# Kernel tuning notes

Measured on AMD Instinct MI355X. Metric: run time of the kernel, lower is better.

Reference implementation:

```python
import jax, jax.numpy as jnp
import numpy as np

NC, NX, NY = 32, 512, 512
N_LOC = 100000


def setup_inputs() -> dict:
    key = jax.random.key(0)
    k1, k2 = jax.random.split(key)
    x = jax.random.normal(k1, (8, NC, NX, NY), dtype=jnp.float32)
    kernel = jnp.zeros((1, NC, NX, NY), dtype=jnp.float32)
    variable_kernel = jax.random.normal(k2, (N_LOC,), dtype=jnp.float32)
    # unique flat indices into the (NC, NX, NY) kernel volume (cluster locations)
    rng = np.random.default_rng(0)
    loc_idx = jnp.asarray(rng.choice(NC * NX * NY, N_LOC, replace=False).astype(np.int64))
    return {"x": x, "kernel": kernel, "variable_kernel": variable_kernel, "loc_idx": loc_idx}


def fill_kernel(kernel, variable_kernel, loc_idx):
    # scatter ReLU'd trainable values into the sparse PSF locations
    k0 = kernel[0].reshape(-1).at[loc_idx].set(jax.nn.relu(variable_kernel))
    return k0.reshape(NC, NX, NY)


def disperse_all_orders(x, k):
    # per-channel circular convolution with the multi-order dispersion PSF,
    # summed over spectral channels onto the sensor: (b, nx, ny)
    Xf = jnp.fft.rfft2(x, axes=(-2, -1))          # (b, nc, nx, ny//2+1)
    Kf = jnp.fft.rfft2(k, axes=(-2, -1))          # (nc, nx, ny//2+1)
    Yf = jnp.sum(Xf * Kf[None], axis=1)           # (b, nx, ny//2+1)
    return jnp.fft.irfft2(Yf, s=(NX, NY), axes=(-2, -1))


def reference(x, kernel, variable_kernel, loc_idx):
    k = fill_kernel(kernel, variable_kernel, loc_idx)
    return disperse_all_orders(x, k)
```

## Files before the change

### kernel.cpp

```cpp
#include <hip/hip_runtime.h>
#include <cstdint>

#define NXX 512
#define NYY 512
#define NCH 32
#define NB  8
#define NU  257
#define IMG_CPLX (NU*NXX)
#define PIX (NXX*NYY)

__device__ __forceinline__ uint32_t f2bf(float f){
  uint32_t u = __float_as_uint(f);
  return (u + 0x7FFFu + ((u >> 16) & 1u)) >> 16;
}
__device__ __forceinline__ float bf2f(uint32_t h){ return __uint_as_float(h << 16); }
__device__ __forceinline__ uint32_t packbf(float re, float im){ return f2bf(re) | (f2bf(im) << 16); }

#define WAIT_LGKM() asm volatile("s_waitcnt lgkmcnt(0)" ::: "memory")

__device__ __forceinline__ void cmul(float& zr, float& zi, float wr, float wi){
  float r = zr*wr - zi*wi;
  zi = zr*wi + zi*wr;
  zr = r;
}

template<int DIR>
__device__ __forceinline__ void bfly8(float* xr, float* xi){
  const float S = 0.70710678118654752440f;
  float er0=xr[0]+xr[4], ei0=xi[0]+xi[4];
  float er1=xr[1]+xr[5], ei1=xi[1]+xi[5];
  float er2=xr[2]+xr[6], ei2=xi[2]+xi[6];
  float er3=xr[3]+xr[7], ei3=xi[3]+xi[7];
  float or0=xr[0]-xr[4], oi0=xi[0]-xi[4];
  float or1=xr[1]-xr[5], oi1=xi[1]-xi[5];
  float or2=xr[2]-xr[6], oi2=xi[2]-xi[6];
  float or3=xr[3]-xr[7], oi3=xi[3]-xi[7];
  float p0r=er0+er2, p0i=ei0+ei2;
  float p1r=er0-er2, p1i=ei0-ei2;
  float q0r=er1+er3, q0i=ei1+ei3;
  float q1r=er1-er3, q1i=ei1-ei3;
  float w4r, w4i;
  if (DIR<0){ w4r=q1i; w4i=-q1r; } else { w4r=-q1i; w4i=q1r; }
  xr[0]=p0r+q0r; xi[0]=p0i+q0i;
  xr[4]=p0r-q0r; xi[4]=p0i-q0i;
  xr[2]=p1r+w4r; xi[2]=p1i+w4i;
  xr[6]=p1r-w4r; xi[6]=p1i-w4i;
  float f1r,f1i,f2r,f2i,f3r,f3i;
  if (DIR<0){
    f1r=S*(or1+oi1); f1i=S*(oi1-or1);
    f2r=oi2;         f2i=-or2;
    f3r=S*(oi3-or3); f3i=-S*(or3+oi3);
  } else {
    f1r=S*(or1-oi1);  f1i=S*(or1+oi1);
    f2r=-oi2;         f2i=or2;
    f3r=-S*(or3+oi3); f3i=S*(or3-oi3);
  }
  float g0r=or0+f2r, g0i=oi0+f2i;
  float g1r=or0-f2r, g1i=oi0-f2i;
  float h0r=f1r+f3r, h0i=f1i+f3i;
  float h1r=f1r-f3r, h1i=f1i-f3i;
  float v4r, v4i;
  if (DIR<0){ v4r=h1i; v4i=-h1r; } else { v4r=-h1i; v4i=h1r; }
  xr[1]=g0r+h0r; xi[1]=g0i+h0i;
  xr[5]=g0r-h0r; xi[5]=g0i-h0i;
  xr[3]=g1r+v4r; xi[3]=g1i+v4i;
  xr[7]=g1r-v4r; xi[7]=g1i-v4i;
}

__device__ __forceinline__ void make_tw(int t, float* t1r, float* t1i, float* t2r, float* t2i){
  const float TP = 6.283185307179586476925f;
  float s, c;
  sincosf(-TP * (float)t * (1.0f/512.0f), &s, &c);
  t1r[0]=1.0f; t1i[0]=0.0f;
  #pragma unroll
  for (int k=1;k<8;k++){ t1r[k]=t1r[k-1]*c - t1i[k-1]*s; t1i[k]=t1r[k-1]*s + t1i[k-1]*c; }
  sincosf(-TP * (float)(t>>3) * (1.0f/64.0f), &s, &c);
  t2r[0]=1.0f; t2i[0]=0.0f;
  #pragma unroll
  for (int k=1;k<8;k++){ t2r[k]=t2r[k-1]*c - t2i[k-1]*s; t2i[k]=t2r[k-1]*s + t2i[k-1]*c; }
}

template<int DIR>
__device__ __forceinline__ void fft512(float* ar, float* ai, float* sre, float* sim, int t,
    const float* t1r, const float* t1i, const float* t2r, const float* t2i){
  bfly8<DIR>(ar, ai);
  #pragma unroll
  for (int k=1;k<8;k++){ cmul(ar[k], ai[k], t1r[k], (DIR<0)? t1i[k] : -t1i[k]); }
  #pragma unroll
  for (int k=0;k<8;k++){ int d = 8*t + k; d += (d>>5); sre[d]=ar[k]; sim[d]=ai[k]; }
  WAIT_LGKM();
  #pragma unroll
  for (int j=0;j<8;j++){ int s2 = t + (j<<6); s2 += (s2>>5); ar[j]=sre[s2]; ai[j]=sim[s2]; }
  WAIT_LGKM();
  bfly8<DIR>(ar, ai);
  #pragma unroll
  for (int k=1;k<8;k++){ cmul(ar[k], ai[k], t2r[k], (DIR<0)? t2i[k] : -t2i[k]); }
  #pragma unroll
  for (int k=0;k<8;k++){ int d = (t&7) + ((t>>3)<<6) + (k<<3); d += (d>>5); sre[d]=ar[k]; sim[d]=ai[k]; }
  WAIT_LGKM();
  #pragma unroll
  for (int j=0;j<8;j++){ int s2 = t + (j<<6); s2 += (s2>>5); ar[j]=sre[s2]; ai[j]=sim[s2]; }
  WAIT_LGKM();
  bfly8<DIR>(ar, ai);
}

__global__ __launch_bounds__(256) void k_zero(uint4* __restrict__ p, int n4){
  int stride = gridDim.x * 256;
  for (int i = blockIdx.x*256 + threadIdx.x; i < n4; i += stride)
    p[i] = make_uint4(0u,0u,0u,0u);
}

__global__ void k_scatter(const float* __restrict__ vk, const int* __restrict__ loc,
                          float* __restrict__ kbuf, int n){
  int i = blockIdx.x*256 + threadIdx.x;
  if (i < n){ float v = vk[i]; kbuf[loc[i]] = v > 0.0f ? v : 0.0f; }
}

__global__ __launch_bounds__(512) void k_p1(const float* __restrict__ src,
                                            uint32_t* __restrict__ dst){
  __shared__ float sre[8][528], sim[8][528];
  __shared__ uint32_t staged[NU*17];
  const int tid = threadIdx.x;
  const int w = tid >> 6, t = tid & 63;
  const int img = blockIdx.x >> 5;
  const int rblock = (blockIdx.x & 31) << 4;
  float t1r[8],t1i[8],t2r[8],t2i[8];
  make_tw(t, t1r,t1i,t2r,t2i);
  const float* rowA = src + (size_t)img*PIX + (size_t)(rblock + 2*w)*NYY;
  float ar[8], ai[8];
  #pragma unroll
  for (int j=0;j<8;j++){ ar[j]=rowA[t+(j<<6)]; ai[j]=rowA[NYY + t + (j<<6)]; }
  fft512<-1>(ar,ai,sre[w],sim[w],t,t1r,t1i,t2r,t2i);
  #pragma unroll
  for (int k=0;k<8;k++){ int d = t+(k<<6); d += (d>>5); sre[w][d]=ar[k]; sim[w][d]=ai[k]; }
  WAIT_LGKM();
  #pragma unroll
  for (int k=0;k<5;k++){
    int u = t + (k<<6);
    if (u < NU){
      int e2 = (512 - u) & 511;
      int du = u + (u>>5), d2 = e2 + (e2>>5);
      float zur=sre[w][du], zui=sim[w][du];
      float zvr=sre[w][d2], zvi=sim[w][d2];
      float Ar=0.5f*(zur+zvr), Ai=0.5f*(zui-zvi);
      float Br=0.5f*(zui+zvi), Bi=0.5f*(zvr-zur);
      staged[u*17 + 2*w]     = packbf(Ar,Ai);
      staged[u*17 + 2*w + 1] = packbf(Br,Bi);
    }
  }
  __syncthreads();
  uint32_t* ob = dst + (size_t)img*IMG_CPLX;
  for (int e = tid; e < NU*16; e += 512){
    int u = e >> 4, il = e & 15;
    ob[(size_t)u*NXX + rblock + il] = staged[u*17 + il];
  }
}

__global__ __launch_bounds__(512) void k_p2k(uint32_t* __restrict__ rtk){
  __shared__ float sre[8][528], sim[8][528];
  const int w = threadIdx.x >> 6, t = threadIdx.x & 63;
  const int fid = blockIdx.x*8 + w;
  const int c = fid / NU, u = fid % NU;
  float t1r[8],t1i[8],t2r[8],t2i[8];
  make_tw(t, t1r,t1i,t2r,t2i);
  uint32_t* col = rtk + (size_t)c*IMG_CPLX + (size_t)u*NXX;
  float ar[8], ai[8];
  #pragma unroll
  for (int j=0;j<8;j++){ uint32_t v = col[t+(j<<6)]; ar[j]=bf2f(v & 0xFFFFu); ai[j]=bf2f(v >> 16); }
  fft512<-1>(ar,ai,sre[w],sim[w],t,t1r,t1i,t2r,t2i);
  #pragma unroll
  for (int k=0;k<8;k++){ col[t+(k<<6)] = packbf(ar[k], ai[k]); }
}

__global__ __launch_bounds__(512) void k_p3(const uint32_t* __restrict__ rtx,
    const uint32_t* __restrict__ rtk, uint32_t* __restrict__ y3, int b0, int gsh){
  __shared__ float sre[8][528], sim[8][528];
  const int w = threadIdx.x >> 6, t = threadIdx.x & 63;
  const int G = 1 << gsh;
  const int u = blockIdx.x * (8 >> gsh) + (w >> gsh);
  const int bl = w & (G-1);
  if (u >= NU) return;
  float t1r[8],t1i[8],t2r[8],t2i[8];
  make_tw(t, t1r,t1i,t2r,t2i);
  float accr[8], acci[8];
  #pragma unroll
  for (int k=0;k<8;k++){ accr[k]=0.0f; acci[k]=0.0f; }
  for (int c=0;c<NCH;c++){
    const uint32_t* xc = rtx + ((size_t)(bl*NCH + c))*IMG_CPLX + (size_t)u*NXX;
    float ar[8], ai[8];
    #pragma unroll
    for (int j=0;j<8;j++){ uint32_t v = xc[t+(j<<6)]; ar[j]=bf2f(v & 0xFFFFu); ai[j]=bf2f(v >> 16); }
    fft512<-1>(ar,ai,sre[w],sim[w],t,t1r,t1i,t2r,t2i);
    const uint32_t* kc = rtk + (size_t)c*IMG_CPLX + (size_t)u*NXX;
    #pragma unroll
    for (int k=0;k<8;k++){
      uint32_t kv = kc[t+(k<<6)];
      float kr=bf2f(kv & 0xFFFFu), ki=bf2f(kv >> 16);
      accr[k] += ar[k]*kr - ai[k]*ki;
      acci[k] += ar[k]*ki + ai[k]*kr;
    }
  }
  const float sc = 1.0f/262144.0f;
  #pragma unroll
  for (int k=0;k<8;k++){ accr[k]*=sc; acci[k]*=sc; }
  fft512<1>(accr,acci,sre[w],sim[w],t,t1r,t1i,t2r,t2i);
  uint32_t* yc = y3 + ((size_t)(b0+bl)*NU + u)*NXX;
  #pragma unroll
  for (int k=0;k<8;k++){ yc[t+(k<<6)] = packbf(accr[k], acci[k]); }
}

__global__ __launch_bounds__(512) void k_p4(const uint32_t* __restrict__ y3,
                                            float* __restrict__ out){
  __shared__ float sre[8][528], sim[8][528];
  __shared__ uint32_t sta[NU*17];
  const int tid = threadIdx.x, w = tid>>6, t = tid&63;
  const int b = blockIdx.x >> 5;
  const int i0 = (blockIdx.x & 31) << 4;
  const uint32_t* yb = y3 + (size_t)b*IMG_CPLX;
  for (int e = tid; e < NU*16; e += 512){
    int u = e >> 4, il = e & 15;
    sta[u*17 + il] = yb[(size_t)u*NXX + i0 + il];
  }
  __syncthreads();
  float t1r[8],t1i[8],t2r[8],t2i[8];
  make_tw(t, t1r,t1i,t2r,t2i);
  float ar[8], ai[8];
  #pragma unroll
  for (int j=0;j<8;j++){
    int e = t + (j<<6);
    if (e <= 256){
      uint32_t pa_ = sta[e*17 + 2*w], pb_ = sta[e*17 + 2*w + 1];
      float Ar=bf2f(pa_&0xFFFFu), Ai=bf2f(pa_>>16);
      float Br=bf2f(pb_&0xFFFFu), Bi=bf2f(pb_>>16);
      ar[j] = Ar - Bi; ai[j] = Ai + Br;
    } else {
      int ep = 512 - e;
      uint32_t pa_ = sta[ep*17 + 2*w], pb_ = sta[ep*17 + 2*w + 1];
      float Ar=bf2f(pa_&0xFFFFu), Ai=bf2f(pa_>>16);
      float Br=bf2f(pb_&0xFFFFu), Bi=bf2f(pb_>>16);
      ar[j] = Ar + Bi; ai[j] = Br - Ai;
    }
  }
  fft512<1>(ar,ai,sre[w],sim[w],t,t1r,t1i,t2r,t2i);
  float* ob = out + (size_t)b*PIX + (size_t)(i0 + 2*w)*NYY;
  #pragma unroll
  for (int k=0;k<8;k++){ int n = t+(k<<6); ob[n]=ar[k]; ob[NYY+n]=ai[k]; }
}

extern "C" void kernel_launch(void* const* d_in, const int* in_sizes, int n_in,
                              void* d_out, int out_size, void* d_ws, size_t ws_size,
                              hipStream_t stream) {
  const float* x  = (const float*)d_in[0];
  const float* vk = (const float*)d_in[2];
  const int*   loc= (const int*)d_in[3];
  float* out = (float*)d_out;
  char* ws = (char*)d_ws;
  const int n_loc = in_sizes[2];

  const size_t kbytes   = (size_t)NCH*PIX*4;
  const size_t imgbytes = (size_t)IMG_CPLX*4;

  float*    kbuf = (float*)ws;
  uint32_t* y3   = (uint32_t*)ws;
  uint32_t* rtk  = (uint32_t*)(ws + kbytes);
  uint32_t* rtx  = rtk + (size_t)NCH*IMG_CPLX;

  int G = 8;
  while (G > 1 && kbytes + (size_t)(NCH + NCH*G)*imgbytes > ws_size) G >>= 1;
  const int gsh = (G==8)?3:((G==4)?2:((G==2)?1:0));

  k_zero<<<2048, 256, 0, stream>>>((uint4*)kbuf, (int)(kbytes/16));
  k_scatter<<<(n_loc+255)/256, 256, 0, stream>>>(vk, loc, kbuf, n_loc);
  k_p1<<<NCH*32, 512, 0, stream>>>(kbuf, rtk);
  k_p2k<<<(NCH*NU)/8, 512, 0, stream>>>(rtk);
  for (int b0 = 0; b0 < NB; b0 += G){
    k_p1<<<G*NCH*32, 512, 0, stream>>>(x + (size_t)b0*NCH*PIX, rtx);
    const int upw = 8 >> gsh;
    const int nwg = (NU + upw - 1) / upw;
    k_p3<<<nwg, 512, 0, stream>>>(rtx, rtk, y3, b0, gsh);
  }
  k_p4<<<NB*32, 512, 0, stream>>>(y3, out);
}
```

Baseline: 210.9 us.

## Split channel loop across waves in k_p3 and widen k_p1 row tiles

The frequency-domain multiply-accumulate kernel now assigns one block per (column, batch) pair. Its eight waves each handle four channels, and an LDS reduction combines them before a single wave performs the inverse column FFT. This exposes far more blocks than the previous layout, where each wave serially looped over all 32 channels. The row FFT kernel now processes 32 rows per block in two passes, giving wider contiguous transposed writes. The cost is extra shared memory for the reduction buffers and an inverse-FFT tail where seven waves sit idle.

```diff
diff --git a/kernel.cpp b/kernel.cpp
--- a/kernel.cpp
+++ b/kernel.cpp
@@ -119,40 +119,45 @@
 __global__ __launch_bounds__(512) void k_p1(const float* __restrict__ src,
                                             uint32_t* __restrict__ dst){
   __shared__ float sre[8][528], sim[8][528];
-  __shared__ uint32_t staged[NU*17];
+  __shared__ uint32_t staged[NU*33];
   const int tid = threadIdx.x;
   const int w = tid >> 6, t = tid & 63;
-  const int img = blockIdx.x >> 5;
-  const int rblock = (blockIdx.x & 31) << 4;
+  const int img = blockIdx.x >> 4;
+  const int rblock = (blockIdx.x & 15) << 5;
   float t1r[8],t1i[8],t2r[8],t2i[8];
   make_tw(t, t1r,t1i,t2r,t2i);
-  const float* rowA = src + (size_t)img*PIX + (size_t)(rblock + 2*w)*NYY;
-  float ar[8], ai[8];
-  #pragma unroll
-  for (int j=0;j<8;j++){ ar[j]=rowA[t+(j<<6)]; ai[j]=rowA[NYY + t + (j<<6)]; }
-  fft512<-1>(ar,ai,sre[w],sim[w],t,t1r,t1i,t2r,t2i);
-  #pragma unroll
-  for (int k=0;k<8;k++){ int d = t+(k<<6); d += (d>>5); sre[w][d]=ar[k]; sim[w][d]=ai[k]; }
-  WAIT_LGKM();
-  #pragma unroll
-  for (int k=0;k<5;k++){
-    int u = t + (k<<6);
-    if (u < NU){
-      int e2 = (512 - u) & 511;
-      int du = u + (u>>5), d2 = e2 + (e2>>5);
-      float zur=sre[w][du], zui=sim[w][du];
-      float zvr=sre[w][d2], zvi=sim[w][d2];
-      float Ar=0.5f*(zur+zvr), Ai=0.5f*(zui-zvi);
-      float Br=0.5f*(zui+zvi), Bi=0.5f*(zvr-zur);
-      staged[u*17 + 2*w]     = packbf(Ar,Ai);
-      staged[u*17 + 2*w + 1] = packbf(Br,Bi);
+  #pragma unroll
+  for (int p=0; p<2; p++){
+    const int il = (w<<2) + (p<<1);
+    const float* rowA = src + (size_t)img*PIX + (size_t)(rblock + il)*NYY;
+    float ar[8], ai[8];
+    #pragma unroll
+    for (int j=0;j<8;j++){ ar[j]=rowA[t+(j<<6)]; ai[j]=rowA[NYY + t + (j<<6)]; }
+    fft512<-1>(ar,ai,sre[w],sim[w],t,t1r,t1i,t2r,t2i);
+    #pragma unroll
+    for (int k=0;k<8;k++){ int d = t+(k<<6); d += (d>>5); sre[w][d]=ar[k]; sim[w][d]=ai[k]; }
+    WAIT_LGKM();
+    #pragma unroll
+    for (int k=0;k<5;k++){
+      int u = t + (k<<6);
+      if (u < NU){
+        int e2 = (512 - u) & 511;
+        int du = u + (u>>5), d2 = e2 + (e2>>5);
+        float zur=sre[w][du], zui=sim[w][du];
+        float zvr=sre[w][d2], zvi=sim[w][d2];
+        float Ar=0.5f*(zur+zvr), Ai=0.5f*(zui-zvi);
+        float Br=0.5f*(zui+zvi), Bi=0.5f*(zvr-zur);
+        staged[u*33 + il]     = packbf(Ar,Ai);
+        staged[u*33 + il + 1] = packbf(Br,Bi);
+      }
     }
+    WAIT_LGKM();
   }
   __syncthreads();
   uint32_t* ob = dst + (size_t)img*IMG_CPLX;
-  for (int e = tid; e < NU*16; e += 512){
-    int u = e >> 4, il = e & 15;
-    ob[(size_t)u*NXX + rblock + il] = staged[u*17 + il];
+  for (int e = tid; e < NU*32; e += 512){
+    int u = e >> 5, il2 = e & 31;
+    ob[(size_t)u*NXX + rblock + il2] = staged[u*33 + il2];
   }
 }
 
@@ -175,38 +180,53 @@
 __global__ __launch_bounds__(512) void k_p3(const uint32_t* __restrict__ rtx,
     const uint32_t* __restrict__ rtk, uint32_t* __restrict__ y3, int b0, int gsh){
   __shared__ float sre[8][528], sim[8][528];
-  const int w = threadIdx.x >> 6, t = threadIdx.x & 63;
-  const int G = 1 << gsh;
-  const int u = blockIdx.x * (8 >> gsh) + (w >> gsh);
-  const int bl = w & (G-1);
-  if (u >= NU) return;
+  __shared__ float redr[8][512], redi[8][512];
+  const int tid = threadIdx.x;
+  const int w = tid >> 6, t = tid & 63;
+  const int u  = blockIdx.x >> gsh;
+  const int bl = blockIdx.x & ((1<<gsh)-1);
   float t1r[8],t1i[8],t2r[8],t2i[8];
   make_tw(t, t1r,t1i,t2r,t2i);
   float accr[8], acci[8];
   #pragma unroll
   for (int k=0;k<8;k++){ accr[k]=0.0f; acci[k]=0.0f; }
-  for (int c=0;c<NCH;c++){
+  #pragma unroll
+  for (int cc=0; cc<4; cc++){
+    const int c = (w<<2) + cc;
     const uint32_t* xc = rtx + ((size_t)(bl*NCH + c))*IMG_CPLX + (size_t)u*NXX;
+    const uint32_t* kc = rtk + (size_t)c*IMG_CPLX + (size_t)u*NXX;
+    uint32_t xv[8], kv[8];
+    #pragma unroll
+    for (int j=0;j<8;j++){ xv[j]=xc[t+(j<<6)]; kv[j]=kc[t+(j<<6)]; }
     float ar[8], ai[8];
     #pragma unroll
-    for (int j=0;j<8;j++){ uint32_t v = xc[t+(j<<6)]; ar[j]=bf2f(v & 0xFFFFu); ai[j]=bf2f(v >> 16); }
+    for (int j=0;j<8;j++){ ar[j]=bf2f(xv[j] & 0xFFFFu); ai[j]=bf2f(xv[j] >> 16); }
     fft512<-1>(ar,ai,sre[w],sim[w],t,t1r,t1i,t2r,t2i);
-    const uint32_t* kc = rtk + (size_t)c*IMG_CPLX + (size_t)u*NXX;
     #pragma unroll
     for (int k=0;k<8;k++){
-      uint32_t kv = kc[t+(k<<6)];
-      float kr=bf2f(kv & 0xFFFFu), ki=bf2f(kv >> 16);
+      float kr=bf2f(kv[k] & 0xFFFFu), ki=bf2f(kv[k] >> 16);
       accr[k] += ar[k]*kr - ai[k]*ki;
       acci[k] += ar[k]*ki + ai[k]*kr;
     }
   }
+  #pragma unroll
+  for (int k=0;k<8;k++){ redr[w][t+(k<<6)] = accr[k]; redi[w][t+(k<<6)] = acci[k]; }
+  __syncthreads();
   const float sc = 1.0f/262144.0f;
-  #pragma unroll
-  for (int k=0;k<8;k++){ accr[k]*=sc; acci[k]*=sc; }
-  fft512<1>(accr,acci,sre[w],sim[w],t,t1r,t1i,t2r,t2i);
-  uint32_t* yc = y3 + ((size_t)(b0+bl)*NU + u)*NXX;
-  #pragma unroll
-  for (int k=0;k<8;k++){ yc[t+(k<<6)] = packbf(accr[k], acci[k]); }
+  float sr=0.0f, si=0.0f;
+  #pragma unroll
+  for (int ww=0; ww<8; ww++){ sr += redr[ww][tid]; si += redi[ww][tid]; }
+  redr[0][tid] = sr*sc; redi[0][tid] = si*sc;
+  __syncthreads();
+  if (w==0){
+    float ar[8], ai[8];
+    #pragma unroll
+    for (int j=0;j<8;j++){ ar[j]=redr[0][t+(j<<6)]; ai[j]=redi[0][t+(j<<6)]; }
+    fft512<1>(ar,ai,sre[0],sim[0],t,t1r,t1i,t2r,t2i);
+    uint32_t* yc = y3 + ((size_t)(b0+bl)*NU + u)*NXX;
+    #pragma unroll
+    for (int k=0;k<8;k++){ yc[t+(k<<6)] = packbf(ar[k], ai[k]); }
+  }
 }
 
 __global__ __launch_bounds__(512) void k_p4(const uint32_t* __restrict__ y3,
@@ -271,13 +291,11 @@
 
   k_zero<<<2048, 256, 0, stream>>>((uint4*)kbuf, (int)(kbytes/16));
   k_scatter<<<(n_loc+255)/256, 256, 0, stream>>>(vk, loc, kbuf, n_loc);
-  k_p1<<<NCH*32, 512, 0, stream>>>(kbuf, rtk);
+  k_p1<<<NCH*16, 512, 0, stream>>>(kbuf, rtk);
   k_p2k<<<(NCH*NU)/8, 512, 0, stream>>>(rtk);
   for (int b0 = 0; b0 < NB; b0 += G){
-    k_p1<<<G*NCH*32, 512, 0, stream>>>(x + (size_t)b0*NCH*PIX, rtx);
-    const int upw = 8 >> gsh;
-    const int nwg = (NU + upw - 1) / upw;
-    k_p3<<<nwg, 512, 0, stream>>>(rtx, rtk, y3, b0, gsh);
+    k_p1<<<G*NCH*16, 512, 0, stream>>>(x + (size_t)b0*NCH*PIX, rtx);
+    k_p3<<<NU<<gsh, 512, 0, stream>>>(rtx, rtk, y3, b0, gsh);
   }
   k_p4<<<NB*32, 512, 0, stream>>>(y3, out);
 }
```

After: 193.0 us. -8.5%, faster.
